# Kernel tuning notes

Hardware: AMD Instinct MI355X
Metric: run time of the kernel (lower is better)

## Reference

```python
import jax, jax.numpy as jnp
import numpy as np

MARGIN = 0.2
NEG_SENTINEL = -1e30


def setup_inputs() -> dict:
    key = jax.random.key(0)
    k1, k2 = jax.random.split(key)
    batch_reprs = jax.random.normal(k1, (4096, 128), dtype=jnp.float32)
    batch_labels = jax.random.randint(k2, (4096,), 0, 512, dtype=jnp.int64 if jax.config.jax_enable_x64 else jnp.int32)
    return {"batch_reprs": batch_reprs, "batch_labels": batch_labels}


def _loss(batch_reprs, batch_labels):
    # class match matrix (self-similarity kept, as in original)
    match = (batch_labels[:, None] == batch_labels[None, :]).astype(batch_reprs.dtype)  # [B,B]

    # pairwise euclidean distance (squared=False), sim = -dist
    sq = jnp.sum(batch_reprs * batch_reprs, axis=1)
    d2 = jnp.maximum(sq[:, None] + sq[None, :] - 2.0 * (batch_reprs @ batch_reprs.T), 0.0)
    zero = (d2 == 0.0).astype(batch_reprs.dtype)
    dist = jnp.sqrt(d2 + zero * 1e-16) * (1.0 - zero)
    sim_hat = -dist + (1.0 - match) * MARGIN  # use_margin=True

    # rank positions via double argsort (descending)
    order = jnp.argsort(-sim_hat, axis=1)
    rank = jnp.argsort(order, axis=1).astype(sim_hat.dtype) + 1.0  # [B,B], 1-based ranks

    k = jnp.sum(match, axis=1, keepdims=True)                      # n_pos per row, [B,1]
    fp = (match < 1.0) & (rank <= k)                               # false positives
    fp_num = jnp.sum(fp, axis=1, keepdims=True).astype(sim_hat.dtype)
    fn = (match > 0.0) & (rank > k)                                # false negatives

    n = sim_hat.shape[1]
    # per-row top-(fp_num) false negatives by sim_hat, vectorized via masked sort
    fn_scores = jnp.where(fn, sim_hat, NEG_SENTINEL)
    idx = jnp.argsort(-fn_scores, axis=1)
    fn_sorted = jnp.take_along_axis(sim_hat, idx, axis=1)
    fn_ranks = jnp.take_along_axis(rank, idx, axis=1)
    fn_mask_sorted = jnp.take_along_axis(fn, idx, axis=1)
    sel = (jnp.arange(n)[None, :] < fp_num) & fn_mask_sorted       # top fp_num entries

    # weighted margins (rows with fp_num==0 contribute 0 automatically)
    fp_term = jnp.sum(jnp.where(fp, sim_hat * (0.5 + (k - rank + 1.0) / k * 0.5), 0.0))
    fn_term = jnp.sum(jnp.where(sel, fn_sorted * (0.5 + (fn_ranks - k) / (n - k) * 0.5), 0.0))
    return fp_term - fn_term


def reference(batch_reprs, batch_labels):
    return _loss(batch_reprs, batch_labels)
```

## Files before the change

kernel.cpp:

```cpp
#include <hip/hip_runtime.h>
#include <cstdint>
#include <cstddef>

#define B 4096
#define D 128
#define MARGIN_F 0.2f
#define CW 256
#define ROWS 16
#define SSTR 4104

typedef short bf16x8 __attribute__((ext_vector_type(8)));
typedef float f32x4 __attribute__((ext_vector_type(4)));
typedef uint32_t u32x4 __attribute__((ext_vector_type(4)));

__device__ __forceinline__ uint32_t xform_key(float f) {
    uint32_t u = __float_as_uint(f);
    return u ^ (uint32_t)((((int32_t)u) >> 31) | 0x80000000);
}
__device__ __forceinline__ float unxform16(uint32_t k16) {
    uint32_t u = k16 << 16;
    u = (u & 0x80000000u) ? (u ^ 0x80000000u) : ~u;
    return __uint_as_float(u);
}
__device__ __forceinline__ unsigned short f2bf(float f) {
    uint32_t u = __float_as_uint(f);
    return (unsigned short)((u + 0x7FFFu + ((u >> 16) & 1u)) >> 16);
}

__global__ __launch_bounds__(256) void prep_kernel(const float* __restrict__ R,
                                                   const int* __restrict__ labels,
                                                   float* __restrict__ sq,
                                                   unsigned short* __restrict__ Rb,
                                                   unsigned long long* __restrict__ mask64,
                                                   float* __restrict__ out) {
    if (blockIdx.x == 0 && threadIdx.x == 0) out[0] = 0.0f;
    int wave = threadIdx.x >> 6;
    int lane = threadIdx.x & 63;
    int row  = blockIdx.x * 4 + wave;
    const float2* R2 = (const float2*)R + (size_t)row * (D / 2);
    float2 v = R2[lane];
    ushort2 o; o.x = f2bf(v.x); o.y = f2bf(v.y);
    *(ushort2*)(Rb + (size_t)row * D + lane * 2) = o;
    float s = v.x * v.x + v.y * v.y;
#pragma unroll
    for (int off = 32; off > 0; off >>= 1) s += __shfl_down(s, off);
    if (lane == 0) sq[row] = s;

    if (threadIdx.x < 32) {
        int p  = blockIdx.x * 32 + threadIdx.x;
        int l  = p >> 6;
        int ln = p & 63;
        unsigned long long m = 0ull;
#pragma unroll
        for (int qq = 0; qq < 8; ++qq) {
            int jb = qq * 512 + ln * 8;
#pragma unroll
            for (int c = 0; c < 8; ++c)
                m |= (unsigned long long)(labels[jb + c] == l) << (qq * 8 + c);
        }
        mask64[(size_t)l * 64 + ln] = m;
    }
}

__global__ __launch_bounds__(1024, 4) void fused_loss(const unsigned short* __restrict__ Rb,
                                                      const float* __restrict__ sq,
                                                      const int* __restrict__ labels,
                                                      const unsigned long long* __restrict__ mask64,
                                                      float* __restrict__ out) {
    __shared__ unsigned short S[ROWS * SSTR];
    __shared__ uint32_t cand_c[ROWS][CW];
    __shared__ int cnt[ROWS];

    const int tid  = threadIdx.x;
    const int wid  = tid >> 6, lane = tid & 63;
    const int q    = lane >> 4, t = lane & 15;
    const int r0   = blockIdx.x * ROWS;

    if (tid < ROWS) cnt[tid] = 0;

    bf16x8 af[4];
    const unsigned short* baseA = Rb + (size_t)(r0 + t) * D + q * 8;
#pragma unroll
    for (int kq = 0; kq < 4; ++kq)
        af[kq] = *(const bf16x8*)(baseA + kq * 32);

    float sqa[4]; int la[4];
#pragma unroll
    for (int rr = 0; rr < 4; ++rr) {
        sqa[rr] = sq[r0 + q * 4 + rr];
        la[rr]  = labels[r0 + q * 4 + rr];
    }

    for (int i = 0; i < 16; i += 2) {
        const int col0 = (wid * 16 + i) * 16 + t;
        const int col1 = col0 + 16;
        const unsigned short* b0 = Rb + (size_t)col0 * D + q * 8;
        const unsigned short* b1 = Rb + (size_t)col1 * D + q * 8;
        bf16x8 f0[4], f1[4];
#pragma unroll
        for (int kq = 0; kq < 4; ++kq) f0[kq] = *(const bf16x8*)(b0 + kq * 32);
#pragma unroll
        for (int kq = 0; kq < 4; ++kq) f1[kq] = *(const bf16x8*)(b1 + kq * 32);
        const float sqc0 = sq[col0], sqc1 = sq[col1];
        const int   lc0  = labels[col0], lc1 = labels[col1];

        f32x4 a0 = (f32x4)0.0f, a1 = (f32x4)0.0f;
#pragma unroll
        for (int kq = 0; kq < 4; ++kq)
            a0 = __builtin_amdgcn_mfma_f32_16x16x32_bf16(af[kq], f0[kq], a0, 0, 0, 0);
#pragma unroll
        for (int kq = 0; kq < 4; ++kq)
            a1 = __builtin_amdgcn_mfma_f32_16x16x32_bf16(af[kq], f1[kq], a1, 0, 0, 0);

#pragma unroll
        for (int rr = 0; rr < 4; ++rr) {
            float d20 = fmaxf(sqa[rr] + sqc0 - 2.0f * a0[rr], 0.0f);
            float di0 = (d20 > 0.0f) ? sqrtf(d20) : 0.0f;
            float s0 = -di0 + ((la[rr] == lc0) ? 0.0f : MARGIN_F);
            S[(q * 4 + rr) * SSTR + col0] =
                (unsigned short)((xform_key(s0) + 0x8000u) >> 16);
            float d21 = fmaxf(sqa[rr] + sqc1 - 2.0f * a1[rr], 0.0f);
            float di1 = (d21 > 0.0f) ? sqrtf(d21) : 0.0f;
            float s1 = -di1 + ((la[rr] == lc1) ? 0.0f : MARGIN_F);
            S[(q * 4 + rr) * SSTR + col1] =
                (unsigned short)((xform_key(s1) + 0x8000u) >> 16);
        }
    }
    __syncthreads();

    float facc = 0.0f;
    {
        const int row  = wid;
        const int grow = r0 + row;
        const int li   = labels[grow];

        const uint64_t mbits = mask64[(size_t)li * 64 + lane];

        u32x4 kv[8];
#pragma unroll
        for (int qq = 0; qq < 8; ++qq)
            kv[qq] = *(u32x4*)(&S[row * SSTR + (qq * 64 + lane) * 8]);

        uint32_t t1 = 0, t2 = 0;
#pragma unroll
        for (int qq = 0; qq < 8; ++qq) {
            uint32_t u[8] = {kv[qq].x & 0xFFFFu, kv[qq].x >> 16,
                             kv[qq].y & 0xFFFFu, kv[qq].y >> 16,
                             kv[qq].z & 0xFFFFu, kv[qq].z >> 16,
                             kv[qq].w & 0xFFFFu, kv[qq].w >> 16};
#pragma unroll
            for (int c = 0; c < 8; ++c) {
                uint32_t mn = min(t1, u[c]);
                t1 = max(t1, u[c]);
                t2 = max(t2, mn);
            }
        }

        int kloc = __popcll(mbits);
#pragma unroll
        for (int off = 32; off > 0; off >>= 1) kloc += __shfl_xor(kloc, off);
        const int k = kloc;
        const float kf = (float)k;

        const int kneed = min(k, 128);
        uint32_t T = 0;
#pragma unroll
        for (int b = 15; b >= 0; --b) {
            uint32_t g = T | (1u << b);
            int c = __popcll(__ballot(t1 >= g)) + __popcll(__ballot(t2 >= g));
            if (c >= kneed) T = g;
        }
        const uint32_t combT = T << 12;

#pragma unroll
        for (int qq = 0; qq < 8; ++qq) {
            uint32_t u[8] = {kv[qq].x & 0xFFFFu, kv[qq].x >> 16,
                             kv[qq].y & 0xFFFFu, kv[qq].y >> 16,
                             kv[qq].z & 0xFFFFu, kv[qq].z >> 16,
                             kv[qq].w & 0xFFFFu, kv[qq].w >> 16};
            int jb = (qq * 64 + lane) * 8;
#pragma unroll
            for (int c = 0; c < 8; ++c) {
                int e = qq * 8 + c;
                uint32_t m = (uint32_t)((mbits >> e) & 1);
                if (u[c] >= T || m) {
                    int p = atomicAdd(&cnt[row], 1);
                    if (p < CW)
                        cand_c[row][p] = (u[c] << 12) | (uint32_t)(4095 - (jb + c)) | (m << 31);
                }
            }
        }
        const int ncand = min(cnt[row], CW);

        for (int s = lane; s < ncand; s += 64) {
            uint32_t cs = cand_c[row][s];
            uint32_t comb = cs & 0x7FFFFFFFu;
            int m = (int)(cs >> 31);
            if (comb >= combT) {
                int c2 = 0;
                for (int c = 0; c < ncand; ++c)
                    c2 += ((cand_c[row][c] & 0x7FFFFFFFu) > comb) ? 1 : 0;
                int rank = 1 + c2;
                float v = unxform16(comb >> 12);
                if (!m && rank <= k)
                    facc += v * (0.5f + ((kf - (float)rank + 1.0f) / kf) * 0.5f);
                else if (m && rank > k)
                    facc -= v * (0.5f + (((float)rank - kf) / (float)(B - k)) * 0.5f);
            }
        }

        uint32_t p0 = 0xFFFFFFFFu, p1 = 0xFFFFFFFFu, p2 = 0xFFFFFFFFu, p3 = 0xFFFFFFFFu;
        int np = 0;
        for (int c = 0; c <= ncand; ++c) {
            bool flushit = (c == ncand);
            if (!flushit) {
                uint32_t cc_ = cand_c[row][c];
                if ((cc_ & 0x80000000u) && (cc_ & 0x7FFFFFFFu) < combT) {
                    uint32_t comb = cc_ & 0x7FFFFFFFu;
                    if (np == 0) p0 = comb; else if (np == 1) p1 = comb;
                    else if (np == 2) p2 = comb; else p3 = comb;
                    ++np;
                    flushit = (np == 4);
                }
            }
            if (flushit && np > 0) {
                int c0 = 0, c1 = 0, c2 = 0, c3 = 0;
#pragma unroll
                for (int qq = 0; qq < 8; ++qq) {
                    uint32_t u[8] = {kv[qq].x & 0xFFFFu, kv[qq].x >> 16,
                                     kv[qq].y & 0xFFFFu, kv[qq].y >> 16,
                                     kv[qq].z & 0xFFFFu, kv[qq].z >> 16,
                                     kv[qq].w & 0xFFFFu, kv[qq].w >> 16};
                    int jb = (qq * 64 + lane) * 8;
#pragma unroll
                    for (int cc = 0; cc < 8; ++cc) {
                        uint32_t comb_e = (u[cc] << 12) | (uint32_t)(4095 - (jb + cc));
                        c0 += (comb_e > p0) ? 1 : 0;
                        c1 += (comb_e > p1) ? 1 : 0;
                        c2 += (comb_e > p2) ? 1 : 0;
                        c3 += (comb_e > p3) ? 1 : 0;
                    }
                }
#pragma unroll
                for (int off = 32; off > 0; off >>= 1) {
                    c0 += __shfl_xor(c0, off); c1 += __shfl_xor(c1, off);
                    c2 += __shfl_xor(c2, off); c3 += __shfl_xor(c3, off);
                }
                if (lane == 0) {
                    int rk[4] = {1 + c0, 1 + c1, 1 + c2, 1 + c3};
                    uint32_t pp[4] = {p0, p1, p2, p3};
                    for (int ii = 0; ii < np; ++ii) {
                        float v = unxform16(pp[ii] >> 12);
                        facc -= v * (0.5f + (((float)rk[ii] - kf) / (float)(B - k)) * 0.5f);
                    }
                }
                p0 = p1 = p2 = p3 = 0xFFFFFFFFu;
                np = 0;
            }
        }
    }

#pragma unroll
    for (int off = 32; off > 0; off >>= 1) facc += __shfl_xor(facc, off);
    if (lane == 0) atomicAdd(out, facc);
}

extern "C" void kernel_launch(void* const* d_in, const int* in_sizes, int n_in,
                              void* d_out, int out_size, void* d_ws, size_t ws_size,
                              hipStream_t stream) {
    const float* R      = (const float*)d_in[0];
    const int*   labels = (const int*)d_in[1];
    float* out = (float*)d_out;

    float*              sq   = (float*)d_ws;
    unsigned short*     Rb   = (unsigned short*)((char*)d_ws + 16 * 1024);
    unsigned long long* mask = (unsigned long long*)((char*)d_ws + 16 * 1024 + 1024 * 1024);

    hipLaunchKernelGGL(prep_kernel, dim3(B / 4), dim3(256), 0, stream,
                       R, labels, sq, Rb, mask, out);
    hipLaunchKernelGGL(fused_loss, dim3(B / ROWS), dim3(1024), 0, stream,
                       Rb, sq, labels, mask, out);
}
```

Baseline: 149.2 us.

## Halve block to 512 threads, two rows per wave, batch 8 FN pivots

The fused loss kernel now runs with 8 waves per block instead of 16. Each wave computes twice as many similarity column tiles and then processes two rows sequentially in the ranking phase. The false-negative rank counting now compares against 8 pivot values per pass instead of 4, so fewer scans over the row's keys are needed. In exchange it uses more registers and serialises the per-row work within a wave, which may reduce latency hiding, especially since the ranking phase is divergent.

```diff
diff --git a/kernel.cpp b/kernel.cpp
--- a/kernel.cpp
+++ b/kernel.cpp
@@ -62,11 +62,11 @@
     }
 }
 
-__global__ __launch_bounds__(1024, 4) void fused_loss(const unsigned short* __restrict__ Rb,
-                                                      const float* __restrict__ sq,
-                                                      const int* __restrict__ labels,
-                                                      const unsigned long long* __restrict__ mask64,
-                                                      float* __restrict__ out) {
+__global__ __launch_bounds__(512) void fused_loss(const unsigned short* __restrict__ Rb,
+                                                  const float* __restrict__ sq,
+                                                  const int* __restrict__ labels,
+                                                  const unsigned long long* __restrict__ mask64,
+                                                  float* __restrict__ out) {
     __shared__ unsigned short S[ROWS * SSTR];
     __shared__ uint32_t cand_c[ROWS][CW];
     __shared__ int cnt[ROWS];
@@ -91,8 +91,8 @@
         la[rr]  = labels[r0 + q * 4 + rr];
     }
 
-    for (int i = 0; i < 16; i += 2) {
-        const int col0 = (wid * 16 + i) * 16 + t;
+    for (int i = 0; i < 32; i += 2) {
+        const int col0 = (wid * 32 + i) * 16 + t;
         const int col1 = col0 + 16;
         const unsigned short* b0 = Rb + (size_t)col0 * D + q * 8;
         const unsigned short* b1 = Rb + (size_t)col1 * D + q * 8;
@@ -129,11 +129,11 @@
     __syncthreads();
 
     float facc = 0.0f;
-    {
-        const int row  = wid;
+
+    for (int rr2 = 0; rr2 < 2; ++rr2) {
+        const int row  = wid * 2 + rr2;
         const int grow = r0 + row;
         const int li   = labels[grow];
-
         const uint64_t mbits = mask64[(size_t)li * 64 + lane];
 
         u32x4 kv[8];
@@ -209,22 +209,29 @@
             }
         }
 
-        uint32_t p0 = 0xFFFFFFFFu, p1 = 0xFFFFFFFFu, p2 = 0xFFFFFFFFu, p3 = 0xFFFFFFFFu;
+        uint32_t pa0, pa1, pa2, pa3, pa4, pa5, pa6, pa7;
+        pa0 = pa1 = pa2 = pa3 = pa4 = pa5 = pa6 = pa7 = 0xFFFFFFFFu;
         int np = 0;
         for (int c = 0; c <= ncand; ++c) {
-            bool flushit = (c == ncand);
-            if (!flushit) {
+            bool fl = (c == ncand);
+            if (!fl) {
                 uint32_t cc_ = cand_c[row][c];
                 if ((cc_ & 0x80000000u) && (cc_ & 0x7FFFFFFFu) < combT) {
                     uint32_t comb = cc_ & 0x7FFFFFFFu;
-                    if (np == 0) p0 = comb; else if (np == 1) p1 = comb;
-                    else if (np == 2) p2 = comb; else p3 = comb;
+                    if      (np == 0) pa0 = comb;
+                    else if (np == 1) pa1 = comb;
+                    else if (np == 2) pa2 = comb;
+                    else if (np == 3) pa3 = comb;
+                    else if (np == 4) pa4 = comb;
+                    else if (np == 5) pa5 = comb;
+                    else if (np == 6) pa6 = comb;
+                    else              pa7 = comb;
                     ++np;
-                    flushit = (np == 4);
-                }
-            }
-            if (flushit && np > 0) {
-                int c0 = 0, c1 = 0, c2 = 0, c3 = 0;
+                    fl = (np == 8);
+                }
+            }
+            if (fl && np > 0) {
+                int c0 = 0, c1 = 0, c2 = 0, c3 = 0, c4 = 0, c5 = 0, c6 = 0, c7 = 0;
 #pragma unroll
                 for (int qq = 0; qq < 8; ++qq) {
                     uint32_t u[8] = {kv[qq].x & 0xFFFFu, kv[qq].x >> 16,
@@ -235,26 +242,33 @@
 #pragma unroll
                     for (int cc = 0; cc < 8; ++cc) {
                         uint32_t comb_e = (u[cc] << 12) | (uint32_t)(4095 - (jb + cc));
-                        c0 += (comb_e > p0) ? 1 : 0;
-                        c1 += (comb_e > p1) ? 1 : 0;
-                        c2 += (comb_e > p2) ? 1 : 0;
-                        c3 += (comb_e > p3) ? 1 : 0;
+                        c0 += (comb_e > pa0) ? 1 : 0;
+                        c1 += (comb_e > pa1) ? 1 : 0;
+                        c2 += (comb_e > pa2) ? 1 : 0;
+                        c3 += (comb_e > pa3) ? 1 : 0;
+                        c4 += (comb_e > pa4) ? 1 : 0;
+                        c5 += (comb_e > pa5) ? 1 : 0;
+                        c6 += (comb_e > pa6) ? 1 : 0;
+                        c7 += (comb_e > pa7) ? 1 : 0;
                     }
                 }
 #pragma unroll
                 for (int off = 32; off > 0; off >>= 1) {
                     c0 += __shfl_xor(c0, off); c1 += __shfl_xor(c1, off);
                     c2 += __shfl_xor(c2, off); c3 += __shfl_xor(c3, off);
+                    c4 += __shfl_xor(c4, off); c5 += __shfl_xor(c5, off);
+                    c6 += __shfl_xor(c6, off); c7 += __shfl_xor(c7, off);
                 }
                 if (lane == 0) {
-                    int rk[4] = {1 + c0, 1 + c1, 1 + c2, 1 + c3};
-                    uint32_t pp[4] = {p0, p1, p2, p3};
+                    int rk[8] = {1 + c0, 1 + c1, 1 + c2, 1 + c3,
+                                 1 + c4, 1 + c5, 1 + c6, 1 + c7};
+                    uint32_t pp[8] = {pa0, pa1, pa2, pa3, pa4, pa5, pa6, pa7};
                     for (int ii = 0; ii < np; ++ii) {
                         float v = unxform16(pp[ii] >> 12);
                         facc -= v * (0.5f + (((float)rk[ii] - kf) / (float)(B - k)) * 0.5f);
                     }
                 }
-                p0 = p1 = p2 = p3 = 0xFFFFFFFFu;
+                pa0 = pa1 = pa2 = pa3 = pa4 = pa5 = pa6 = pa7 = 0xFFFFFFFFu;
                 np = 0;
             }
         }
@@ -278,6 +292,6 @@
 
     hipLaunchKernelGGL(prep_kernel, dim3(B / 4), dim3(256), 0, stream,
                        R, labels, sq, Rb, mask, out);
-    hipLaunchKernelGGL(fused_loss, dim3(B / ROWS), dim3(1024), 0, stream,
+    hipLaunchKernelGGL(fused_loss, dim3(B / ROWS), dim3(512), 0, stream,
                        Rb, sq, labels, mask, out);
 }
```

Result: faster. 139.1 us (-6.8%).
